# Kernel tuning notes

Measured on AMD Instinct MI355X. Metric: run time of the kernel, lower is better.

The kernel has to match this reference:

```python
import jax, jax.numpy as jnp
import numpy as np

DIM, N_HEADS, N_KV, HEAD_DIM = 4096, 32, 8, 128
N_REP = N_HEADS // N_KV
MAX_BS, MAX_SEQ = 2, 2048
ROPE_THETA = 500000.0


def setup_inputs() -> dict:
    key = jax.random.key(0)
    ks = jax.random.split(key, 6)
    b, s = 2, 2048
    x = jax.random.normal(ks[0], (b, s, DIM), dtype=jnp.float32)
    # weights stored like nn.Linear: [out, in]
    sc = 1.0 / np.sqrt(DIM)
    wq = jax.random.normal(ks[1], (N_HEADS * HEAD_DIM, DIM), dtype=jnp.float32) * sc
    wk = jax.random.normal(ks[2], (N_KV * HEAD_DIM, DIM), dtype=jnp.float32) * sc
    wv = jax.random.normal(ks[3], (N_KV * HEAD_DIM, DIM), dtype=jnp.float32) * sc
    wo = jax.random.normal(ks[4], (DIM, N_HEADS * HEAD_DIM), dtype=jnp.float32) * sc
    # rotary tables (real/imag of freq_complex)
    t = jnp.arange(s, dtype=jnp.float32)
    inv = ROPE_THETA ** (-jnp.arange(0, HEAD_DIM, 2, dtype=jnp.float32) / HEAD_DIM)
    ang = t[:, None] * inv[None, :]  # [s, head_dim/2]
    freqs_cos = jnp.cos(ang)
    freqs_sin = jnp.sin(ang)
    cache_k = jnp.zeros((MAX_BS, MAX_SEQ, N_KV, HEAD_DIM), dtype=jnp.float32)
    cache_v = jnp.zeros((MAX_BS, MAX_SEQ, N_KV, HEAD_DIM), dtype=jnp.float32)
    return {"x": x, "wq": wq, "wk": wk, "wv": wv, "wo": wo,
            "freqs_cos": freqs_cos, "freqs_sin": freqs_sin,
            "cache_k": cache_k, "cache_v": cache_v, "start_pos": 0}


def _apply_rope(t, cos, sin):
    # t: [b, s, h, hd]; complex rotation over adjacent pairs
    b, s, h, hd = t.shape
    t2 = t.reshape(b, s, h, hd // 2, 2)
    t0, t1 = t2[..., 0], t2[..., 1]
    c = cos[None, :, None, :]
    sn = sin[None, :, None, :]
    o0 = t0 * c - t1 * sn
    o1 = t0 * sn + t1 * c
    return jnp.stack([o0, o1], axis=-1).reshape(b, s, h, hd)


def reference(x, wq, wk, wv, wo, freqs_cos, freqs_sin, cache_k, cache_v, start_pos):
    b, s, _ = x.shape
    xq = (x @ wq.T).reshape(b, s, N_HEADS, HEAD_DIM)
    xk = (x @ wk.T).reshape(b, s, N_KV, HEAD_DIM)
    xv = (x @ wv.T).reshape(b, s, N_KV, HEAD_DIM)
    xq = _apply_rope(xq, freqs_cos, freqs_sin)
    xk = _apply_rope(xk, freqs_cos, freqs_sin)
    # KV-cache append at start_pos
    cache_k = jax.lax.dynamic_update_slice(cache_k, xk, (0, start_pos, 0, 0))
    cache_v = jax.lax.dynamic_update_slice(cache_v, xv, (0, start_pos, 0, 0))
    kv_len = start_pos + s
    keys = cache_k[:b, :kv_len]   # [b, kv, n_kv, hd]
    vals = cache_v[:b, :kv_len]
    # GQA: group query heads instead of repeating K/V (same math as repeat_kv)
    q = xq.reshape(b, s, N_KV, N_REP, HEAD_DIM)
    scores = jnp.einsum('bsgrd,btgd->bgrst', q, keys) / np.sqrt(HEAD_DIM)
    # causal mask: query i (absolute pos start_pos+i) attends to j <= start_pos+i
    qpos = start_pos + jnp.arange(s)
    kpos = jnp.arange(kv_len)
    mask = kpos[None, :] <= qpos[:, None]  # [s, kv]
    scores = jnp.where(mask[None, None, None], scores, -jnp.inf)
    probs = jax.nn.softmax(scores, axis=-1)
    out = jnp.einsum('bgrst,btgd->bsgrd', probs, vals).reshape(b, s, N_HEADS * HEAD_DIM)
    return out @ wo.T
```

## Files before the change

kernel.cpp:

```cpp
#include <hip/hip_runtime.h>
#include <stdint.h>

typedef unsigned short ushort_t;
typedef short v8s __attribute__((ext_vector_type(8)));
typedef short v4s __attribute__((ext_vector_type(4)));
typedef float v4f __attribute__((ext_vector_type(4)));
typedef unsigned int uint32;

#define DIM   4096
#define NH    32
#define NKV   8
#define HD    128
#define SEQ   2048
#define BATCH 2
#define NTOK  (BATCH * SEQ)
#define QKVN  (NH * HD + 2 * NKV * HD)
#define KOFF  (NH * HD)
#define VOFF  (NH * HD + NKV * HD)

__device__ __forceinline__ ushort_t f2bf(float f) {
    uint32 u = __float_as_uint(f);
    u += 0x7fff + ((u >> 16) & 1);
    return (ushort_t)(u >> 16);
}
__device__ __forceinline__ float bf2f(ushort_t h) {
    return __uint_as_float(((uint32)h) << 16);
}
__device__ __forceinline__ void gl2lds16(const void* g, void* l) {
    __builtin_amdgcn_global_load_lds(
        (const __attribute__((address_space(1))) uint32*)g,
        (__attribute__((address_space(3))) uint32*)l, 16, 0, 0);
}
#if __has_builtin(__builtin_amdgcn_exp2f)
__device__ __forceinline__ float fast_exp2(float x) { return __builtin_amdgcn_exp2f(x); }
#else
__device__ __forceinline__ float fast_exp2(float x) { return exp2f(x); }
#endif

#if !defined(__HIP_DEVICE_COMPILE__)
__host__ __device__ static inline v4f MFMA_B16_K16(v4s a, v4s b, v4f c) {
    (void)a; (void)b; return c;
}
#elif __has_builtin(__builtin_amdgcn_mfma_f32_16x16x16_bf16)
#define MFMA_B16_K16(A, B, C) __builtin_amdgcn_mfma_f32_16x16x16_bf16(A, B, C, 0, 0, 0)
#elif __has_builtin(__builtin_amdgcn_mfma_f32_16x16x16bf16_1k)
#define MFMA_B16_K16(A, B, C) __builtin_amdgcn_mfma_f32_16x16x16bf16_1k(A, B, C, 0, 0, 0)
#else
#error "no 16x16x16 bf16 MFMA builtin on device"
#endif

__global__ void cvt_f32_bf16(const float* __restrict__ src,
                             ushort_t* __restrict__ dst, int n4) {
    int i = blockIdx.x * blockDim.x + threadIdx.x;
    if (i >= n4) return;
    float4 v = ((const float4*)src)[i];
    uint32 lo = ((uint32)f2bf(v.y) << 16) | f2bf(v.x);
    uint32 hi = ((uint32)f2bf(v.w) << 16) | f2bf(v.z);
    ((uint2*)dst)[i] = make_uint2(lo, hi);
}

template <int OUT_BF16>
__global__ __launch_bounds__(512, 2) void gemm_bt8(const ushort_t* __restrict__ A,
                                                   const ushort_t* __restrict__ B,
                                                   float* __restrict__ Cf,
                                                   ushort_t* __restrict__ Cb,
                                                   int M, int N, int K) {
    __shared__ ushort_t sm[2][2][16384];
    const int t = threadIdx.x;
    const int w = t >> 6, lane = t & 63;
    const int g8 = lane >> 4, l16 = lane & 15;
    const int wr = w >> 2, wc = w & 3;

    const int gx = gridDim.x;
    const int nwg = gx * gridDim.y;
    const int wg0 = blockIdx.y * gx + blockIdx.x;
    const int swz = (wg0 & 7) * (nwg >> 3) + (wg0 >> 3);
    const int bm = swz % gx, bn = swz / gx;

    const ushort_t* Ab = A + (size_t)bm * 256 * K;
    const ushort_t* Bb = B + (size_t)bn * 256 * K;

    const int prt = t >> 3;
    const int gg  = (t & 7) ^ (prt & 7);
    const int rA0 = prt,                              rA1 = prt + 128;
    const int rB0 = ((prt >> 5) << 6) + (prt & 31),   rB1 = rB0 + 128;

    const int pgk  = g8 ^ (l16 & 7);
    const int aoff = (wr * 64 + l16) * 64;
    const int boff = (wc * 32 + l16) * 64;

#define STAGE_A(buf, ah, k0)                                                   \
  do {                                                                         \
    gl2lds16(&Ab[(size_t)(rA0 + (ah) * 64) * K + (k0) + gg * 8],               \
             &sm[buf][0][(ah) * 8192 + t * 8]);                                \
    gl2lds16(&Ab[(size_t)(rA1 + (ah) * 64) * K + (k0) + gg * 8],               \
             &sm[buf][0][(ah) * 8192 + 4096 + t * 8]);                         \
  } while (0)
#define STAGE_B(buf, bh, k0)                                                   \
  do {                                                                         \
    gl2lds16(&Bb[(size_t)(rB0 + (bh) * 32) * K + (k0) + gg * 8],               \
             &sm[buf][1][(bh) * 8192 + t * 8]);                                \
    gl2lds16(&Bb[(size_t)(rB1 + (bh) * 32) * K + (k0) + gg * 8],               \
             &sm[buf][1][(bh) * 8192 + 4096 + t * 8]);                         \
  } while (0)
#define LD_A(dst, buf, ihi)                                                    \
  do {                                                                         \
    _Pragma("unroll") for (int i_ = 0; i_ < 4; ++i_) {                         \
      (dst)[i_ * 2 + 0] = *(const v8s*)&sm[buf][0][(ihi) * 8192 + aoff + i_ * 1024 + pgk * 8];       \
      (dst)[i_ * 2 + 1] = *(const v8s*)&sm[buf][0][(ihi) * 8192 + aoff + i_ * 1024 + (pgk ^ 4) * 8]; \
    }                                                                          \
  } while (0)
#define LD_B(dst, buf, jhi)                                                    \
  do {                                                                         \
    _Pragma("unroll") for (int j_ = 0; j_ < 2; ++j_) {                         \
      (dst)[j_ * 2 + 0] = *(const v8s*)&sm[buf][1][(jhi) * 8192 + boff + j_ * 1024 + pgk * 8];       \
      (dst)[j_ * 2 + 1] = *(const v8s*)&sm[buf][1][(jhi) * 8192 + boff + j_ * 1024 + (pgk ^ 4) * 8]; \
    }                                                                          \
  } while (0)
#define MM(IHI, JHI, AF, BF)                                                   \
  do {                                                                         \
    __builtin_amdgcn_s_setprio(1);                                             \
    _Pragma("unroll") for (int k_ = 0; k_ < 2; ++k_)                           \
      _Pragma("unroll") for (int i_ = 0; i_ < 4; ++i_)                         \
        _Pragma("unroll") for (int j_ = 0; j_ < 2; ++j_)                       \
          acc[(IHI) * 4 + i_][(JHI) * 2 + j_] =                                \
              __builtin_amdgcn_mfma_f32_16x16x32_bf16(                         \
                  (AF)[i_ * 2 + k_], (BF)[j_ * 2 + k_],                        \
                  acc[(IHI) * 4 + i_][(JHI) * 2 + j_], 0, 0, 0);               \
    __builtin_amdgcn_s_setprio(0);                                             \
  } while (0)

#define TILE_BODY(T, BF, BL, BH)                                               \
  do {                                                                         \
    const int Tp1 = (T) + 1, Tp2 = (T) + 2;                                    \
              \
    LD_A(af, BF, 0);                                                           \
    LD_B(BH, BF, 1);                                                           \
    if (Tp1 < nk) STAGE_B((BF) ^ 1, 1, Tp1 << 6);                              \
    MM(0, 0, af, BL);                                                          \
    __builtin_amdgcn_s_barrier();                                              \
                                             \
    if (Tp2 < nk) STAGE_A(BF, 0, Tp2 << 6);                                    \
    MM(0, 1, af, BH);                                                          \
    __builtin_amdgcn_s_barrier();                                              \
                                             \
    LD_A(af, BF, 1);                                                           \
    if (Tp2 < nk) STAGE_B(BF, 0, Tp2 << 6);                                    \
    MM(1, 1, af, BH);                                                          \
    __builtin_amdgcn_s_barrier();                                              \
          \
    if (Tp2 < nk) STAGE_A(BF, 1, Tp2 << 6);                                    \
    if ((T) < nk - 2) { asm volatile("s_waitcnt vmcnt(6)" ::: "memory"); }     \
    else              { asm volatile("s_waitcnt vmcnt(0)" ::: "memory"); }     \
    __builtin_amdgcn_s_barrier();                                              \
    if (Tp1 < nk) LD_B(BH, (BF) ^ 1, 0);     \
    MM(1, 0, af, BL);                                                          \
            \
  } while (0)

    v4f acc[8][4];
    v4f z = {0.f, 0.f, 0.f, 0.f};
#pragma unroll
    for (int i = 0; i < 8; i++)
#pragma unroll
        for (int j = 0; j < 4; j++) acc[i][j] = z;
    v8s af[8], b0[4], b1[4];

    const int nk = K >> 6;

    STAGE_A(0, 0, 0);  STAGE_B(0, 0, 0);  STAGE_A(0, 1, 0);  STAGE_B(0, 1, 0);
    STAGE_A(1, 0, 64); STAGE_B(1, 0, 64); STAGE_A(1, 1, 64);
    asm volatile("s_waitcnt vmcnt(6)" ::: "memory");
    __builtin_amdgcn_s_barrier();
    LD_B(b0, 0, 0);

    for (int T = 0; T < nk; T += 2) {
        TILE_BODY(T, 0, b0, b1);
        TILE_BODY(T + 1, 1, b1, b0);
    }

#undef STAGE_A
#undef STAGE_B
#undef LD_A
#undef LD_B
#undef MM
#undef TILE_BODY

    const int rowb = bm * 256 + wr * 128;
    const int colb = bn * 256 + wc * 64;
#pragma unroll
    for (int i = 0; i < 8; i++)
#pragma unroll
        for (int j = 0; j < 4; j++)
#pragma unroll
            for (int r = 0; r < 4; r++) {
                int row = rowb + i * 16 + g8 * 4 + r;
                int col = colb + j * 16 + l16;
                float v = acc[i][j][r];
                if (OUT_BF16)
                    Cb[(size_t)row * N + col] = f2bf(v);
                else
                    Cf[(size_t)row * N + col] = v;
            }
}

__global__ __launch_bounds__(256) void rope_reorg(const ushort_t* __restrict__ qkv,
                                                  const float* __restrict__ fc,
                                                  const float* __restrict__ fs,
                                                  ushort_t* __restrict__ Qo,
                                                  ushort_t* __restrict__ Ko) {
    const int tok = blockIdx.x;
    const int bb = tok >> 11, s = tok & 2047;
    const ushort_t* base = qkv + (size_t)tok * QKVN;
    const int t = threadIdx.x;
    const float qscale = 0.08838834764831845f * 1.4426950408889634f;
    uint32* Qw = (uint32*)Qo;
    uint32* Kw = (uint32*)Ko;
#pragma unroll
    for (int i = 0; i < 8; ++i) {
        int p = i * 256 + t;
        int hh = p >> 6, pi = p & 63;
        float c = fc[s * 64 + pi], sn = fs[s * 64 + pi];
        uint32 u = *(const uint32*)&base[hh * 128 + 2 * pi];
        float t0 = bf2f((ushort_t)(u & 0xffff));
        float t1 = bf2f((ushort_t)(u >> 16));
        float o0 = (t0 * c - t1 * sn) * qscale;
        float o1 = (t0 * sn + t1 * c) * qscale;
        size_t dst = (((size_t)bb * NH + hh) * SEQ + s) * HD + 2 * pi;
        Qw[dst >> 1] = ((uint32)f2bf(o1) << 16) | f2bf(o0);
    }
#pragma unroll
    for (int i = 0; i < 2; ++i) {
        int p = i * 256 + t;
        int hh = p >> 6, pi = p & 63;
        float c = fc[s * 64 + pi], sn = fs[s * 64 + pi];
        uint32 u = *(const uint32*)&base[KOFF + hh * 128 + 2 * pi];
        float t0 = bf2f((ushort_t)(u & 0xffff));
        float t1 = bf2f((ushort_t)(u >> 16));
        float o0 = t0 * c - t1 * sn;
        float o1 = t0 * sn + t1 * c;
        size_t dst = (((size_t)bb * NKV + hh) * SEQ + s) * HD + 2 * pi;
        Kw[dst >> 1] = ((uint32)f2bf(o1) << 16) | f2bf(o0);
    }
}

__global__ __launch_bounds__(256) void v_transpose(const ushort_t* __restrict__ qkv,
                                                   ushort_t* __restrict__ Vt) {
    __shared__ ushort_t tile[64][136];
    const int st = blockIdx.x, kvh = blockIdx.y, bb = blockIdx.z;
    const int t = threadIdx.x;
    const int s0 = st * 64;
#pragma unroll
    for (int i = 0; i < 4; ++i) {
        int c = i * 256 + t;
        int r = c >> 4, col8 = (c & 15) * 8;
        int tok = (bb << 11) + s0 + r;
        *(v8s*)&tile[r][col8] =
            *(const v8s*)&qkv[(size_t)tok * QKVN + VOFF + kvh * 128 + col8];
    }
    __syncthreads();
#pragma unroll
    for (int i = 0; i < 4; ++i) {
        int c = i * 256 + t;
        int d = c >> 3, s8 = (c & 7) * 8;
        ushort_t tmp[8];
#pragma unroll
        for (int j = 0; j < 8; j++) tmp[j] = tile[s8 + j][d];
        *(v8s*)&Vt[(((size_t)bb * NKV + kvh) * HD + d) * SEQ + s0 + s8] =
            *(v8s*)tmp;
    }
}

__global__ __launch_bounds__(512, 4) void attn_kernel(const ushort_t* __restrict__ Q,
                                                      const ushort_t* __restrict__ Kc,
                                                      const ushort_t* __restrict__ Vt,
                                                      ushort_t* __restrict__ Out) {
    __shared__ ushort_t Ks[2 * 64 * 128];
    __shared__ ushort_t Vs[3 * 128 * 64];
    const int qtb = gridDim.x - 1 - blockIdx.x;
    const int h = blockIdx.y, bb = blockIdx.z;
    const int kvh = h >> 2;
    const int t = threadIdx.x, w = t >> 6, lane = t & 63;
    const int g8 = lane >> 4, l16 = lane & 15;
    const int R = qtb * 128 + w * 16;
    const int qrow = R + l16;

    const size_t qb = (((size_t)bb * NH + h) * SEQ + R) * HD;
    v8s qf[4];
#pragma unroll
    for (int ks = 0; ks < 4; ++ks)
        qf[ks] = *(const v8s*)&Q[qb + (size_t)l16 * HD + ks * 32 + g8 * 8];

    int kadr[4], vadr[4];
#pragma unroll
    for (int ks = 0; ks < 4; ++ks)
        kadr[ks] = l16 * 128 + (((ks * 4 + g8) ^ l16)) * 8;
#pragma unroll
    for (int j = 0; j < 4; ++j)
        vadr[j] = l16 * 64 + (((j * 2 + (g8 >> 1)) ^ (l16 & 7)) * 8) + (g8 & 1) * 4;

    float m_i = -3.0e38f, l_i = 0.f;
    v4f z = {0.f, 0.f, 0.f, 0.f};
    v4f o[8];
#pragma unroll
    for (int n = 0; n < 8; n++) o[n] = z;

    v4s pjp[4];
    float alo_p[4] = {1.f, 1.f, 1.f, 1.f};
    int skip_p = 1;

    const ushort_t* Kbase = Kc + ((size_t)bb * NKV + kvh) * SEQ * HD;
    const ushort_t* Vbase = Vt + ((size_t)bb * NKV + kvh) * HD * SEQ;

#define STAGE_K(kb, kt)                                                        \
  do {                                                                         \
    const ushort_t* Kt_ = Kbase + (size_t)(kt) * 64 * HD;                      \
    _Pragma("unroll") for (int i_ = 0; i_ < 2; ++i_) {                         \
      int c_ = i_ * 512 + t;                                                   \
      int r_ = c_ >> 4, cc_ = (c_ & 15) ^ (r_ & 15);                           \
      gl2lds16(&Kt_[r_ * 128 + cc_ * 8], &Ks[(kb) * 8192 + c_ * 8]);           \
    }                                                                          \
  } while (0)
#define STAGE_V(vb, kt)                                                        \
  do {                                                                         \
    _Pragma("unroll") for (int i_ = 0; i_ < 2; ++i_) {                         \
      int c_ = i_ * 512 + t;                                                   \
      int d_ = c_ >> 3, cc_ = (c_ & 7) ^ (d_ & 7);                             \
      gl2lds16(&Vbase[(size_t)d_ * SEQ + (kt) * 64 + cc_ * 8],                 \
               &Vs[(vb) * 8192 + c_ * 8]);                                     \
    }                                                                          \
  } while (0)

    const int nkt = 2 * qtb + 2;
    STAGE_K(0, 0); STAGE_V(0, 0);
    asm volatile("s_waitcnt vmcnt(0)" ::: "memory");
    __builtin_amdgcn_s_barrier();

    for (int kt = 0; kt < nkt; ++kt) {
        const int kb = kt & 1;
        const int vbp = (kt + 2) % 3;
        const int k0 = kt * 64;
        if (kt + 1 < nkt) {
            STAGE_K(kb ^ 1, kt + 1);
            STAGE_V((kt + 1) % 3, kt + 1);
            asm volatile("s_waitcnt vmcnt(4)" ::: "memory");
        } else {
            asm volatile("s_waitcnt vmcnt(0)" ::: "memory");
        }
        __builtin_amdgcn_s_barrier();

        v4f s[4];
#pragma unroll
        for (int j = 0; j < 4; j++) s[j] = z;
        __builtin_amdgcn_s_setprio(1);
#pragma unroll
        for (int j = 0; j < 4; j++)
#pragma unroll
            for (int ks = 0; ks < 4; ks++) {
                const v8s kb_ = *(const v8s*)&Ks[kb * 8192 + j * 2048 + kadr[ks]];
                s[j] = __builtin_amdgcn_mfma_f32_16x16x32_bf16(kb_, qf[ks], s[j], 0, 0, 0);
            }
        __builtin_amdgcn_s_setprio(0);

        if (kt) {
            if (!skip_p) {
#pragma unroll
                for (int n = 0; n < 8; n++)
#pragma unroll
                    for (int r = 0; r < 4; r++) o[n][r] *= alo_p[r];
            }
            __builtin_amdgcn_s_setprio(1);
#pragma unroll
            for (int j = 0; j < 4; j++)
#pragma unroll
                for (int n = 0; n < 8; n++) {
                    const v4s vb_ = *(const v4s*)&Vs[vbp * 8192 + n * 1024 + vadr[j]];
                    o[n] = MFMA_B16_K16(pjp[j], vb_, o[n]);
                }
            __builtin_amdgcn_s_setprio(0);
        }

        if (kt >= 2 * qtb) {
#pragma unroll
            for (int j = 0; j < 4; j++)
#pragma unroll
                for (int r = 0; r < 4; r++) {
                    int key = k0 + j * 16 + g8 * 4 + r;
                    if (key > qrow) s[j][r] = -3.0e38f;
                }
        }

        float mx = fmaxf(fmaxf(s[0][0], s[0][1]), fmaxf(s[0][2], s[0][3]));
#pragma unroll
        for (int j = 1; j < 4; j++)
            mx = fmaxf(mx, fmaxf(fmaxf(s[j][0], s[j][1]), fmaxf(s[j][2], s[j][3])));
        mx = fmaxf(mx, __shfl_xor(mx, 16, 64));
        mx = fmaxf(mx, __shfl_xor(mx, 32, 64));

        const int skip = __all(mx - m_i <= 8.0f);
        float alpha = 1.f;
        if (!skip) {
            float mnew = fmaxf(m_i, mx);
            alpha = fast_exp2(m_i - mnew);
            m_i = mnew;
        }

        float sum = 0.f;
#pragma unroll
        for (int j = 0; j < 4; j++)
#pragma unroll
            for (int r = 0; r < 4; r++) {
                float p = fast_exp2(s[j][r] - m_i);
                sum += p;
                pjp[j][r] = (short)f2bf(p);
            }
        sum += __shfl_xor(sum, 16, 64);
        sum += __shfl_xor(sum, 32, 64);
        l_i = l_i * alpha + sum;

        if (!skip) {
#pragma unroll
            for (int r = 0; r < 4; r++) alo_p[r] = __shfl(alpha, g8 * 4 + r, 64);
        }
        skip_p = skip;

        __builtin_amdgcn_s_barrier();
    }

    {
        const int vbl = (nkt + 2) % 3;
        if (!skip_p) {
#pragma unroll
            for (int n = 0; n < 8; n++)
#pragma unroll
                for (int r = 0; r < 4; r++) o[n][r] *= alo_p[r];
        }
#pragma unroll
        for (int j = 0; j < 4; j++)
#pragma unroll
            for (int n = 0; n < 8; n++) {
                const v4s vb_ = *(const v4s*)&Vs[vbl * 8192 + n * 1024 + vadr[j]];
                o[n] = MFMA_B16_K16(pjp[j], vb_, o[n]);
            }
    }
#undef STAGE_K
#undef STAGE_V

    float lo[4];
#pragma unroll
    for (int r = 0; r < 4; r++) lo[r] = __shfl(l_i, g8 * 4 + r, 64);
#pragma unroll
    for (int n = 0; n < 8; n++)
#pragma unroll
        for (int r = 0; r < 4; r++) {
            int row = R + g8 * 4 + r;
            int col = n * 16 + l16;
            Out[(((size_t)bb * SEQ + row) * NH + h) * HD + col] = f2bf(o[n][r] / lo[r]);
        }
}

extern "C" void kernel_launch(void* const* d_in, const int* in_sizes, int n_in,
                              void* d_out, int out_size, void* d_ws, size_t ws_size,
                              hipStream_t stream) {
    const float* x  = (const float*)d_in[0];
    const float* wq = (const float*)d_in[1];
    const float* wk = (const float*)d_in[2];
    const float* wv = (const float*)d_in[3];
    const float* wo = (const float*)d_in[4];
    const float* fc = (const float*)d_in[5];
    const float* fs = (const float*)d_in[6];
    float* out = (float*)d_out;

    ushort_t* ws = (ushort_t*)d_ws;
    size_t off = 0;
    ushort_t* xb    = ws + off; off += (size_t)NTOK * DIM;
    ushort_t* wqkvb = ws + off; off += (size_t)QKVN * DIM;
    ushort_t* wob   = ws + off; off += (size_t)DIM * DIM;
    ushort_t* qkv   = ws + off; off += (size_t)NTOK * QKVN;
    ushort_t* Qb    = ws + off; off += (size_t)BATCH * NH * SEQ * HD;
    ushort_t* Kb    = ws + off; off += (size_t)BATCH * NKV * SEQ * HD;
    ushort_t* Vt    = ws + off; off += (size_t)BATCH * NKV * HD * SEQ;
    ushort_t* attn_out = xb;

    cvt_f32_bf16<<<(NTOK * DIM / 4) / 256, 256, 0, stream>>>(x, xb, NTOK * DIM / 4);
    cvt_f32_bf16<<<(DIM * DIM / 4) / 256, 256, 0, stream>>>(wq, wqkvb, DIM * DIM / 4);
    cvt_f32_bf16<<<(NKV * HD * DIM / 4) / 256, 256, 0, stream>>>(
        wk, wqkvb + (size_t)KOFF * DIM, NKV * HD * DIM / 4);
    cvt_f32_bf16<<<(NKV * HD * DIM / 4) / 256, 256, 0, stream>>>(
        wv, wqkvb + (size_t)VOFF * DIM, NKV * HD * DIM / 4);
    cvt_f32_bf16<<<(DIM * DIM / 4) / 256, 256, 0, stream>>>(wo, wob, DIM * DIM / 4);

    dim3 g1(NTOK / 256, QKVN / 256);
    gemm_bt8<1><<<g1, 512, 0, stream>>>(xb, wqkvb, nullptr, qkv, NTOK, QKVN, DIM);

    rope_reorg<<<NTOK, 256, 0, stream>>>(qkv, fc, fs, Qb, Kb);
    dim3 gv(SEQ / 64, NKV, BATCH);
    v_transpose<<<gv, 256, 0, stream>>>(qkv, Vt);

    dim3 ga(SEQ / 128, NH, BATCH);
    attn_kernel<<<ga, 512, 0, stream>>>(Qb, Kb, Vt, attn_out);

    dim3 g2(NTOK / 256, DIM / 256);
    gemm_bt8<0><<<g2, 512, 0, stream>>>(attn_out, wob, out, nullptr, NTOK, DIM, DIM);
}
```

Measured before the change: 782.4 us.

## Drop LDS staging in attention; read K/V directly from global per wave

```diff
diff --git a/kernel.cpp b/kernel.cpp
--- a/kernel.cpp
+++ b/kernel.cpp
@@ -275,8 +275,6 @@
                                                       const ushort_t* __restrict__ Kc,
                                                       const ushort_t* __restrict__ Vt,
                                                       ushort_t* __restrict__ Out) {
-    __shared__ ushort_t Ks[2 * 64 * 128];
-    __shared__ ushort_t Vs[3 * 128 * 64];
     const int qtb = gridDim.x - 1 - blockIdx.x;
     const int h = blockIdx.y, bb = blockIdx.z;
     const int kvh = h >> 2;
@@ -291,14 +289,6 @@
     for (int ks = 0; ks < 4; ++ks)
         qf[ks] = *(const v8s*)&Q[qb + (size_t)l16 * HD + ks * 32 + g8 * 8];
 
-    int kadr[4], vadr[4];
-#pragma unroll
-    for (int ks = 0; ks < 4; ++ks)
-        kadr[ks] = l16 * 128 + (((ks * 4 + g8) ^ l16)) * 8;
-#pragma unroll
-    for (int j = 0; j < 4; ++j)
-        vadr[j] = l16 * 64 + (((j * 2 + (g8 >> 1)) ^ (l16 & 7)) * 8) + (g8 & 1) * 4;
-
     float m_i = -3.0e38f, l_i = 0.f;
     v4f z = {0.f, 0.f, 0.f, 0.f};
     v4f o[8];
@@ -310,44 +300,13 @@
     int skip_p = 1;
 
     const ushort_t* Kbase = Kc + ((size_t)bb * NKV + kvh) * SEQ * HD;
-    const ushort_t* Vbase = Vt + ((size_t)bb * NKV + kvh) * HD * SEQ;
-
-#define STAGE_K(kb, kt)                                                        \
-  do {                                                                         \
-    const ushort_t* Kt_ = Kbase + (size_t)(kt) * 64 * HD;                      \
-    _Pragma("unroll") for (int i_ = 0; i_ < 2; ++i_) {                         \
-      int c_ = i_ * 512 + t;                                                   \
-      int r_ = c_ >> 4, cc_ = (c_ & 15) ^ (r_ & 15);                           \
-      gl2lds16(&Kt_[r_ * 128 + cc_ * 8], &Ks[(kb) * 8192 + c_ * 8]);           \
-    }                                                                          \
-  } while (0)
-#define STAGE_V(vb, kt)                                                        \
-  do {                                                                         \
-    _Pragma("unroll") for (int i_ = 0; i_ < 2; ++i_) {                         \
-      int c_ = i_ * 512 + t;                                                   \
-      int d_ = c_ >> 3, cc_ = (c_ & 7) ^ (d_ & 7);                             \
-      gl2lds16(&Vbase[(size_t)d_ * SEQ + (kt) * 64 + cc_ * 8],                 \
-               &Vs[(vb) * 8192 + c_ * 8]);                                     \
-    }                                                                          \
-  } while (0)
-
-    const int nkt = 2 * qtb + 2;
-    STAGE_K(0, 0); STAGE_V(0, 0);
-    asm volatile("s_waitcnt vmcnt(0)" ::: "memory");
-    __builtin_amdgcn_s_barrier();
-
+    const ushort_t* Vl = Vt + ((size_t)bb * NKV + kvh) * HD * SEQ
+                            + (size_t)l16 * SEQ + g8 * 4;
+
+    const int nkt = (R >> 6) + 1;
     for (int kt = 0; kt < nkt; ++kt) {
-        const int kb = kt & 1;
-        const int vbp = (kt + 2) % 3;
         const int k0 = kt * 64;
-        if (kt + 1 < nkt) {
-            STAGE_K(kb ^ 1, kt + 1);
-            STAGE_V((kt + 1) % 3, kt + 1);
-            asm volatile("s_waitcnt vmcnt(4)" ::: "memory");
-        } else {
-            asm volatile("s_waitcnt vmcnt(0)" ::: "memory");
-        }
-        __builtin_amdgcn_s_barrier();
+        const ushort_t* Kt = Kbase + (size_t)(k0 + l16) * HD + g8 * 8;
 
         v4f s[4];
 #pragma unroll
@@ -357,12 +316,13 @@
         for (int j = 0; j < 4; j++)
 #pragma unroll
             for (int ks = 0; ks < 4; ks++) {
-                const v8s kb_ = *(const v8s*)&Ks[kb * 8192 + j * 2048 + kadr[ks]];
+                const v8s kb_ = *(const v8s*)&Kt[(size_t)(j * 16) * HD + ks * 32];
                 s[j] = __builtin_amdgcn_mfma_f32_16x16x32_bf16(kb_, qf[ks], s[j], 0, 0, 0);
             }
         __builtin_amdgcn_s_setprio(0);
 
         if (kt) {
+            const int kp = k0 - 64;
             if (!skip_p) {
 #pragma unroll
                 for (int n = 0; n < 8; n++)
@@ -374,13 +334,13 @@
             for (int j = 0; j < 4; j++)
 #pragma unroll
                 for (int n = 0; n < 8; n++) {
-                    const v4s vb_ = *(const v4s*)&Vs[vbp * 8192 + n * 1024 + vadr[j]];
+                    const v4s vb_ = *(const v4s*)&Vl[(size_t)(n * 16) * SEQ + kp + j * 16];
                     o[n] = MFMA_B16_K16(pjp[j], vb_, o[n]);
                 }
             __builtin_amdgcn_s_setprio(0);
         }
 
-        if (kt >= 2 * qtb) {
+        if (kt == nkt - 1) {
 #pragma unroll
             for (int j = 0; j < 4; j++)
 #pragma unroll
@@ -423,12 +383,10 @@
             for (int r = 0; r < 4; r++) alo_p[r] = __shfl(alpha, g8 * 4 + r, 64);
         }
         skip_p = skip;
-
-        __builtin_amdgcn_s_barrier();
     }
 
     {
-        const int vbl = (nkt + 2) % 3;
+        const int kp = (nkt - 1) * 64;
         if (!skip_p) {
 #pragma unroll
             for (int n = 0; n < 8; n++)
@@ -439,12 +397,10 @@
         for (int j = 0; j < 4; j++)
 #pragma unroll
             for (int n = 0; n < 8; n++) {
-                const v4s vb_ = *(const v4s*)&Vs[vbl * 8192 + n * 1024 + vadr[j]];
+                const v4s vb_ = *(const v4s*)&Vl[(size_t)(n * 16) * SEQ + kp + j * 16];
                 o[n] = MFMA_B16_K16(pjp[j], vb_, o[n]);
             }
     }
-#undef STAGE_K
-#undef STAGE_V
 
     float lo[4];
 #pragma unroll
```

Measured after the change: 1.872 ms. 139% more time.
